# Performance work log

Hardware: AMD Instinct MI355X
Metric: run time of the kernel (lower is better)

The kernel has to match this reference:

```python
import jax, jax.numpy as jnp
import numpy as np

B, T, D_MODEL, H, DH = 4, 2048, 768, 12, 64


def _rope_tables(T, dh):
    # standard rotary frequencies, (T, dh//2)
    inv_freq = 1.0 / (10000.0 ** (np.arange(0, dh, 2, dtype=np.float32) / dh))
    t = np.arange(T, dtype=np.float32)
    ang = np.outer(t, inv_freq)  # (T, dh//2)
    return jnp.asarray(np.cos(ang)), jnp.asarray(np.sin(ang))


def setup_inputs() -> dict:
    key = jax.random.key(0)
    ks = jax.random.split(key, 5)
    scale = 1.0 / np.sqrt(D_MODEL)
    x = jax.random.normal(ks[0], (B, T, D_MODEL), dtype=jnp.float32)
    wq = jax.random.normal(ks[1], (D_MODEL, D_MODEL), dtype=jnp.float32) * scale
    wk = jax.random.normal(ks[2], (D_MODEL, D_MODEL), dtype=jnp.float32) * scale
    wv = jax.random.normal(ks[3], (D_MODEL, D_MODEL), dtype=jnp.float32) * scale
    wo = jax.random.normal(ks[4], (D_MODEL, D_MODEL), dtype=jnp.float32) * scale
    rope_cos, rope_sin = _rope_tables(T, DH)
    return {"x": x, "rope_cos": rope_cos, "rope_sin": rope_sin,
            "wq": wq, "wk": wk, "wv": wv, "wo": wo}


def _apply_rope(x, cos, sin):
    # x: (B, H, T, DH), cos/sin: (T, DH//2) -> interleaved rotation
    t = x.shape[2]
    c = cos[:t][None, None]  # (1,1,T,DH//2)
    s = sin[:t][None, None]
    x1 = x[..., ::2]
    x2 = x[..., 1::2]
    return jnp.stack([x1 * c - x2 * s, x1 * s + x2 * c], axis=-1).reshape(x.shape)


def reference(x, rope_cos, rope_sin, wq, wk, wv, wo):
    b, t, _ = x.shape
    # Linear (torch nn.Linear: y = x @ W.T), split heads -> (B,H,T,DH)
    q = (x @ wq.T).reshape(b, t, H, DH).transpose(0, 2, 1, 3)
    k = (x @ wk.T).reshape(b, t, H, DH).transpose(0, 2, 1, 3)
    v = (x @ wv.T).reshape(b, t, H, DH).transpose(0, 2, 1, 3)
    q = _apply_rope(q, rope_cos, rope_sin)
    k = _apply_rope(k, rope_cos, rope_sin)
    scores = jnp.einsum("bhqd,bhkd->bhqk", q, k) * (DH ** -0.5)
    causal = jnp.tril(jnp.ones((t, t), dtype=bool))  # (T,T)
    scores = jnp.where(causal[None, None], scores, -jnp.inf)
    attn = jax.nn.softmax(scores, axis=-1)
    out = jnp.einsum("bhqk,bhkd->bhqd", attn, v)
    out = out.transpose(0, 2, 1, 3).reshape(b, t, H * DH)
    return out @ wo.T
```

## Files before the change

### kernel.cpp

```cpp
#include <hip/hip_runtime.h>
#include <hip/hip_bf16.h>
#include <math.h>

#define B_ 4
#define T_ 2048
#define DM 768
#define H_ 12
#define DH 64

typedef __attribute__((ext_vector_type(4))) float f32x4;
typedef __attribute__((ext_vector_type(8))) short s16x8;

typedef const __attribute__((address_space(1))) void* gas1_t;
typedef __attribute__((address_space(3))) void* las3_t;

__device__ __forceinline__ ushort f2b(float f) {
  union { float f; unsigned u; } v; v.f = f;
  unsigned u = v.u;
  u += 0x7fffu + ((u >> 16) & 1u);
  return (ushort)(u >> 16);
}
__device__ __forceinline__ unsigned cvt_pk_bf16(float lo, float hi) {
  unsigned r;
  asm("v_cvt_pk_bf16_f32 %0, %1, %2" : "=v"(r) : "v"(lo), "v"(hi));
  return r;
}

__global__ void cvt_all(const float* __restrict__ x,
                        const float* __restrict__ wq, const float* __restrict__ wk,
                        const float* __restrict__ wv, const float* __restrict__ wo,
                        const float* __restrict__ rc, const float* __restrict__ rs,
                        ushort* __restrict__ xb, ushort* __restrict__ wqkv,
                        ushort* __restrict__ wob, float2* __restrict__ cs2) {
  const int bid = blockIdx.x, t = threadIdx.x;
  if (bid < 6144) {
    int i = bid * 256 + t;
    float4 v = ((const float4*)x)[i];
    ushort4 o;
    o.x = f2b(v.x); o.y = f2b(v.y); o.z = f2b(v.z); o.w = f2b(v.w);
    ((ushort4*)xb)[i] = o;
  } else if (bid < 8448) {
    int i = (bid - 6144) * 256 + t;
    int which = i / 147456, j = i - which * 147456;
    const float* src = which == 0 ? wq : which == 1 ? wk : which == 2 ? wv : wo;
    ushort* dst = which < 3 ? wqkv + (size_t)which * 589824 : wob;
    float4 v = ((const float4*)src)[j];
    ushort4 o;
    o.x = f2b(v.x); o.y = f2b(v.y); o.z = f2b(v.z); o.w = f2b(v.w);
    ((ushort4*)dst)[j] = o;
  } else {
    int i = (bid - 8448) * 256 + t;
    cs2[i] = make_float2(rc[i], rs[i]);
  }
}

__global__ __launch_bounds__(256, 3) void gemm_qkv(
    const ushort* __restrict__ A, const ushort* __restrict__ Bw,
    const float2* __restrict__ cs2,
    ushort* __restrict__ Qb, ushort* __restrict__ Kb, ushort* __restrict__ Vt) {
  const int K = 768;
  __shared__ ushort As[128 * 64];
  __shared__ ushort Bs[192 * 64];
  const int bid = blockIdx.x;
  const int xcd = bid & 7;
  const int jj = bid >> 3;
  const int mloc = jj / 12, nn0 = jj - mloc * 12;
  const int m0 = (xcd * 8 + mloc) * 128, n0 = nn0 * 192;
  const int tid = threadIdx.x;
  const int wave = tid >> 6, lane = tid & 63;
  const int wm = (wave >> 1) * 64, wn = (wave & 1) * 96;
  const int quad = lane >> 4, l16 = lane & 15;
  const int tr = tid >> 3;
  const int scb = (tid & 7) ^ (tr & 7);
  const int swz = l16 & 7;

  f32x4 acc[4][6] = {};

  const ushort* ga = A + (size_t)(m0 + tr) * K + scb * 8;
  const ushort* gb = Bw + (size_t)(n0 + tr) * K + scb * 8;

  for (int k0 = 0; k0 < K; k0 += 64) {
#pragma unroll
    for (int p = 0; p < 4; p++)
      __builtin_amdgcn_global_load_lds((gas1_t)(ga + (size_t)(p * 32) * K + k0),
                                       (las3_t)(As + p * 2048 + tid * 8), 16, 0, 0);
#pragma unroll
    for (int p = 0; p < 6; p++)
      __builtin_amdgcn_global_load_lds((gas1_t)(gb + (size_t)(p * 32) * K + k0),
                                       (las3_t)(Bs + p * 2048 + tid * 8), 16, 0, 0);
    __syncthreads();
#pragma unroll
    for (int kk = 0; kk < 2; kk++) {
      s16x8 af[4], bf[6];
#pragma unroll
      for (int i = 0; i < 4; i++) {
        const ushort* ar = As + (wm + i * 16 + l16) * 64;
        af[i] = *(const s16x8*)(ar + (((kk * 4 + quad) ^ swz) * 8));
      }
#pragma unroll
      for (int n = 0; n < 6; n++) {
        const ushort* br = Bs + (wn + n * 16 + l16) * 64;
        bf[n] = *(const s16x8*)(br + (((kk * 4 + quad) ^ swz) * 8));
      }
#pragma unroll
      for (int i = 0; i < 4; i++)
#pragma unroll
        for (int n = 0; n < 6; n++)
          acc[i][n] = __builtin_amdgcn_mfma_f32_16x16x32_bf16(af[i], bf[n], acc[i][n], 0, 0, 0);
    }
    __syncthreads();
  }

  const int sec = n0 / 768;
  if (sec < 2) {
    ushort* dst = sec == 0 ? Qb : Kb;
#pragma unroll
    for (int i = 0; i < 4; i++) {
      int row0 = m0 + wm + i * 16 + quad * 4;
#pragma unroll
      for (int nt = 0; nt < 6; nt++) {
        int col = n0 + wn + nt * 16 + l16;
        int nv = col - sec * 768;
        int h = nv >> 6, d = nv & 63;
        int ip = (d >> 1) & 31;
        float sgn = (d & 1) ? 1.f : -1.f;
#pragma unroll
        for (int r = 0; r < 4; r++) {
          int rrow = row0 + r;
          int t = rrow & (T_ - 1), bb = rrow >> 11;
          float v = acc[i][nt][r];
          float partner = __shfl_xor(v, 1);
          float2 cs = cs2[t * 32 + ip];
          float out = fmaf(v, cs.x, sgn * partner * cs.y);
          dst[((size_t)(bb * H_ + h) * T_ + t) * DH + d] = f2b(out);
        }
      }
    }
  } else {
#pragma unroll
    for (int i = 0; i < 4; i++) {
      int row0 = m0 + wm + i * 16 + quad * 4;
      int t0 = row0 & (T_ - 1), b = row0 >> 11;
#pragma unroll
      for (int nt = 0; nt < 6; nt++) {
        int col = n0 + wn + nt * 16 + l16;
        int nv = col - 1536;
        int h = nv >> 6, d = nv & 63;
        ushort4 pk;
        pk.x = f2b(acc[i][nt][0]); pk.y = f2b(acc[i][nt][1]);
        pk.z = f2b(acc[i][nt][2]); pk.w = f2b(acc[i][nt][3]);
        *(ushort4*)(Vt + ((size_t)(b * H_ + h) * DH + d) * T_ + t0) = pk;
      }
    }
  }
}

__global__ __launch_bounds__(256, 3) void gemm_out(
    const ushort* __restrict__ A, const ushort* __restrict__ Bw, float* __restrict__ C) {
  const int K = 768, N = 768;
  __shared__ ushort As[128 * 64];
  __shared__ ushort Bs[64 * 64];
  const int bid = blockIdx.x;
  const int xcd = bid & 7;
  const int jj = bid >> 3;
  const int mloc = jj / 12, nn0 = jj - mloc * 12;
  const int m0 = (xcd * 8 + mloc) * 128, n0 = nn0 * 64;
  const int tid = threadIdx.x;
  const int wave = tid >> 6, lane = tid & 63;
  const int wm = (wave >> 1) * 64, wn = (wave & 1) * 32;
  const int quad = lane >> 4, l16 = lane & 15;
  const int tr = tid >> 3;
  const int scb = (tid & 7) ^ (tr & 7);
  const int swz = l16 & 7;

  f32x4 acc[4][2] = {};

  const ushort* ga = A + (size_t)(m0 + tr) * K + scb * 8;
  const ushort* gb = Bw + (size_t)(n0 + tr) * K + scb * 8;

  for (int k0 = 0; k0 < K; k0 += 64) {
#pragma unroll
    for (int p = 0; p < 4; p++)
      __builtin_amdgcn_global_load_lds((gas1_t)(ga + (size_t)(p * 32) * K + k0),
                                       (las3_t)(As + p * 2048 + tid * 8), 16, 0, 0);
#pragma unroll
    for (int p = 0; p < 2; p++)
      __builtin_amdgcn_global_load_lds((gas1_t)(gb + (size_t)(p * 32) * K + k0),
                                       (las3_t)(Bs + p * 2048 + tid * 8), 16, 0, 0);
    __syncthreads();
#pragma unroll
    for (int kk = 0; kk < 2; kk++) {
      s16x8 af[4], bf[2];
#pragma unroll
      for (int i = 0; i < 4; i++) {
        const ushort* ar = As + (wm + i * 16 + l16) * 64;
        af[i] = *(const s16x8*)(ar + (((kk * 4 + quad) ^ swz) * 8));
      }
#pragma unroll
      for (int n = 0; n < 2; n++) {
        const ushort* br = Bs + (wn + n * 16 + l16) * 64;
        bf[n] = *(const s16x8*)(br + (((kk * 4 + quad) ^ swz) * 8));
      }
#pragma unroll
      for (int i = 0; i < 4; i++)
#pragma unroll
        for (int n = 0; n < 2; n++)
          acc[i][n] = __builtin_amdgcn_mfma_f32_16x16x32_bf16(af[i], bf[n], acc[i][n], 0, 0, 0);
    }
    __syncthreads();
  }

#pragma unroll
  for (int i = 0; i < 4; i++) {
    int row = m0 + wm + i * 16 + quad * 4;
#pragma unroll
    for (int n = 0; n < 2; n++) {
      int col = n0 + wn + n * 16 + l16;
#pragma unroll
      for (int r = 0; r < 4; r++)
        C[(size_t)(row + r) * N + col] = acc[i][n][r];
    }
  }
}

#define EXP2SCALE 0.18033688f
#define EXP2OFF  17.312340f
__global__ __launch_bounds__(256, 3) void attn(const ushort* __restrict__ Qb, const ushort* __restrict__ Kb,
                                               const ushort* __restrict__ Vt, ushort* __restrict__ Ob) {
  const int bh = blockIdx.x;
  const int p = blockIdx.y;
  const int tid = threadIdx.x, wave = tid >> 6, lane = tid & 63;
  const int quad = lane >> 4, l16 = lane & 15;
  const int b = bh / H_, h = bh % H_;
  const ushort* Qp = Qb + (size_t)bh * T_ * DH;
  const ushort* Kp = Kb + (size_t)bh * T_ * DH;
  const ushort* Vp = Vt + (size_t)bh * DH * T_;

  __shared__ ushort Ks[2][64 * 64];
  __shared__ ushort Vs[2][64 * 64];
  __shared__ ushort P[4][16][72];

  const int srow = tid >> 3;
  const int scbK = (tid & 7) ^ (srow & 7);
  const int swz = (l16 & 7);

#pragma unroll
  for (int phase = 0; phase < 2; phase++) {
    const int tile = phase ? (31 - p) : p;
    const int qb = tile * 64 + wave * 16;

    s16x8 aq0, aq1;
    {
      const ushort* qp = Qp + (size_t)(qb + l16) * DH + quad * 8;
      aq0 = *(const s16x8*)qp;
      aq1 = *(const s16x8*)(qp + 32);
    }
    f32x4 o[4] = {};
    float rsum = 0.f;
    const int ntile = tile + 1;

    __syncthreads();
    {
      const int kv0 = 0;
      __builtin_amdgcn_global_load_lds((gas1_t)(Kp + (size_t)(kv0 + srow) * DH + scbK * 8),
                                       (las3_t)(Ks[0] + tid * 8), 16, 0, 0);
      __builtin_amdgcn_global_load_lds((gas1_t)(Kp + (size_t)(kv0 + srow + 32) * DH + scbK * 8),
                                       (las3_t)(Ks[0] + 2048 + tid * 8), 16, 0, 0);
      __builtin_amdgcn_global_load_lds((gas1_t)(Vp + (size_t)srow * T_ + kv0 + scbK * 8),
                                       (las3_t)(Vs[0] + tid * 8), 16, 0, 0);
      __builtin_amdgcn_global_load_lds((gas1_t)(Vp + (size_t)(srow + 32) * T_ + kv0 + scbK * 8),
                                       (las3_t)(Vs[0] + 2048 + tid * 8), 16, 0, 0);
    }

    for (int c = 0; c < ntile; c++) {
      const int kv0 = c * 64;
      const int cur = c & 1;
      __syncthreads();
      if (c + 1 < ntile) {
        const int kv1 = kv0 + 64, nxt = cur ^ 1;
        __builtin_amdgcn_global_load_lds((gas1_t)(Kp + (size_t)(kv1 + srow) * DH + scbK * 8),
                                         (las3_t)(Ks[nxt] + tid * 8), 16, 0, 0);
        __builtin_amdgcn_global_load_lds((gas1_t)(Kp + (size_t)(kv1 + srow + 32) * DH + scbK * 8),
                                         (las3_t)(Ks[nxt] + 2048 + tid * 8), 16, 0, 0);
        __builtin_amdgcn_global_load_lds((gas1_t)(Vp + (size_t)srow * T_ + kv1 + scbK * 8),
                                         (las3_t)(Vs[nxt] + tid * 8), 16, 0, 0);
        __builtin_amdgcn_global_load_lds((gas1_t)(Vp + (size_t)(srow + 32) * T_ + kv1 + scbK * 8),
                                         (las3_t)(Vs[nxt] + 2048 + tid * 8), 16, 0, 0);
      }

      s16x8 kf[4][2];
#pragma unroll
      for (int nt = 0; nt < 4; nt++) {
        const ushort* kr = Ks[cur] + (nt * 16 + l16) * 64;
        kf[nt][0] = *(const s16x8*)(kr + ((quad ^ swz) * 8));
        kf[nt][1] = *(const s16x8*)(kr + (((4 + quad) ^ swz) * 8));
      }
      s16x8 bv[4][2];
#pragma unroll
      for (int dt = 0; dt < 4; dt++) {
        const ushort* vr = Vs[cur] + (dt * 16 + l16) * 64;
        bv[dt][0] = *(const s16x8*)(vr + ((quad ^ swz) * 8));
        bv[dt][1] = *(const s16x8*)(vr + (((4 + quad) ^ swz) * 8));
      }

      f32x4 s[4] = {};
#pragma unroll
      for (int nt = 0; nt < 4; nt++) {
        s[nt] = __builtin_amdgcn_mfma_f32_16x16x32_bf16(kf[nt][0], aq0, s[nt], 0, 0, 0);
        s[nt] = __builtin_amdgcn_mfma_f32_16x16x32_bf16(kf[nt][1], aq1, s[nt], 0, 0, 0);
      }
      if (c < tile) {
#pragma unroll
        for (int nt = 0; nt < 4; nt++) {
          float p0 = __builtin_amdgcn_exp2f(fmaf(s[nt][0], EXP2SCALE, -EXP2OFF));
          float p1 = __builtin_amdgcn_exp2f(fmaf(s[nt][1], EXP2SCALE, -EXP2OFF));
          float p2 = __builtin_amdgcn_exp2f(fmaf(s[nt][2], EXP2SCALE, -EXP2OFF));
          float p3 = __builtin_amdgcn_exp2f(fmaf(s[nt][3], EXP2SCALE, -EXP2OFF));
          rsum += (p0 + p1) + (p2 + p3);
          uint2 pk;
          pk.x = cvt_pk_bf16(p0, p1);
          pk.y = cvt_pk_bf16(p2, p3);
          *(uint2*)&P[wave][l16][nt * 16 + quad * 4] = pk;
        }
      } else {
        int qi = qb + l16;
#pragma unroll
        for (int nt = 0; nt < 4; nt++) {
          int kvb = kv0 + nt * 16 + quad * 4;
          float pv[4];
#pragma unroll
          for (int r = 0; r < 4; r++)
            pv[r] = (kvb + r <= qi) ? __builtin_amdgcn_exp2f(fmaf(s[nt][r], EXP2SCALE, -EXP2OFF)) : 0.f;
          rsum += (pv[0] + pv[1]) + (pv[2] + pv[3]);
          uint2 pk;
          pk.x = cvt_pk_bf16(pv[0], pv[1]);
          pk.y = cvt_pk_bf16(pv[2], pv[3]);
          *(uint2*)&P[wave][l16][nt * 16 + quad * 4] = pk;
        }
      }
      s16x8 ap0 = *(const s16x8*)&P[wave][l16][quad * 8];
      s16x8 ap1 = *(const s16x8*)&P[wave][l16][32 + quad * 8];
#pragma unroll
      for (int dt = 0; dt < 4; dt++) {
        o[dt] = __builtin_amdgcn_mfma_f32_16x16x32_bf16(ap0, bv[dt][0], o[dt], 0, 0, 0);
        o[dt] = __builtin_amdgcn_mfma_f32_16x16x32_bf16(ap1, bv[dt][1], o[dt], 0, 0, 0);
      }
    }

    rsum += __shfl_xor(rsum, 16);
    rsum += __shfl_xor(rsum, 32);
#pragma unroll
    for (int r = 0; r < 4; r++) {
      float inv = 1.0f / __shfl(rsum, quad * 4 + r);
      int q = qb + quad * 4 + r;
#pragma unroll
      for (int dt = 0; dt < 4; dt++)
        Ob[(size_t)(b * T_ + q) * DM + h * 64 + dt * 16 + l16] = f2b(o[dt][r] * inv);
    }
  }
}

extern "C" void kernel_launch(void* const* d_in, const int* in_sizes, int n_in,
                              void* d_out, int out_size, void* d_ws, size_t ws_size,
                              hipStream_t stream) {
  const float* x = (const float*)d_in[0];
  const float* rc = (const float*)d_in[1];
  const float* rs = (const float*)d_in[2];
  const float* wq = (const float*)d_in[3];
  const float* wk = (const float*)d_in[4];
  const float* wv = (const float*)d_in[5];
  const float* wo = (const float*)d_in[6];

  char* ws = (char*)d_ws;
  ushort* xb   = (ushort*)(ws);
  ushort* wqkv = (ushort*)(ws + 12582912);
  ushort* wob  = (ushort*)(ws + 16121856);
  float2* cs2  = (float2*)(ws + 17301504);
  ushort* Qb   = (ushort*)(ws + 17825792);
  ushort* Kb   = (ushort*)(ws + 30408704);
  ushort* Vt   = (ushort*)(ws + 42991616);
  ushort* Ob   = (ushort*)(ws + 55574528);

  cvt_all<<<8704, 256, 0, stream>>>(x, wq, wk, wv, wo, rc, rs, xb, wqkv, wob, cs2);

  gemm_qkv<<<768, 256, 0, stream>>>(xb, wqkv, cs2, Qb, Kb, Vt);

  attn<<<dim3(48, 16), 256, 0, stream>>>(Qb, Kb, Vt, Ob);

  gemm_out<<<768, 256, 0, stream>>>(Ob, wob, (float*)d_out);
}
```

Measured before the change: 193.4 us.

## Fuse paired causal query tiles into one KV sweep sharing K/V loads

The attention kernel previously processed its two paired query tiles (p and 31-p) in two sequential phases, each streaming K/V from global memory. Now a single KV loop serves both tiles: each loaded K/V block and its LDS fragments feed tile B every iteration and tile A while c <= tileA. This cuts the global-to-LDS traffic and barriers for the shorter tile. The cost is more live registers (two Q fragments, two accumulators), which may pressure occupancy under the 3-blocks launch bound.

```diff
diff --git a/kernel.cpp b/kernel.cpp
--- a/kernel.cpp
+++ b/kernel.cpp
@@ -240,90 +240,92 @@
   __shared__ ushort Vs[2][64 * 64];
   __shared__ ushort P[4][16][72];
 
+  const int tileA = p, tileB = 31 - p;
+  const int qbA = tileA * 64 + wave * 16;
+  const int qbB = tileB * 64 + wave * 16;
+
+  s16x8 aqA0, aqA1, aqB0, aqB1;
+  {
+    const ushort* qp = Qp + (size_t)(qbA + l16) * DH + quad * 8;
+    aqA0 = *(const s16x8*)qp;
+    aqA1 = *(const s16x8*)(qp + 32);
+    const ushort* qp2 = Qp + (size_t)(qbB + l16) * DH + quad * 8;
+    aqB0 = *(const s16x8*)qp2;
+    aqB1 = *(const s16x8*)(qp2 + 32);
+  }
+  f32x4 oA[4] = {}, oB[4] = {};
+  float rsA = 0.f, rsB = 0.f;
+
+  const int ntile = 32 - p;
   const int srow = tid >> 3;
   const int scbK = (tid & 7) ^ (srow & 7);
   const int swz = (l16 & 7);
 
-#pragma unroll
-  for (int phase = 0; phase < 2; phase++) {
-    const int tile = phase ? (31 - p) : p;
-    const int qb = tile * 64 + wave * 16;
-
-    s16x8 aq0, aq1;
+  {
+    const int kv0 = 0;
+    __builtin_amdgcn_global_load_lds((gas1_t)(Kp + (size_t)(kv0 + srow) * DH + scbK * 8),
+                                     (las3_t)(Ks[0] + tid * 8), 16, 0, 0);
+    __builtin_amdgcn_global_load_lds((gas1_t)(Kp + (size_t)(kv0 + srow + 32) * DH + scbK * 8),
+                                     (las3_t)(Ks[0] + 2048 + tid * 8), 16, 0, 0);
+    __builtin_amdgcn_global_load_lds((gas1_t)(Vp + (size_t)srow * T_ + kv0 + scbK * 8),
+                                     (las3_t)(Vs[0] + tid * 8), 16, 0, 0);
+    __builtin_amdgcn_global_load_lds((gas1_t)(Vp + (size_t)(srow + 32) * T_ + kv0 + scbK * 8),
+                                     (las3_t)(Vs[0] + 2048 + tid * 8), 16, 0, 0);
+  }
+
+  for (int c = 0; c < ntile; c++) {
+    const int kv0 = c * 64;
+    const int cur = c & 1;
+    __syncthreads();
+    if (c + 1 < ntile) {
+      const int kv1 = kv0 + 64, nxt = cur ^ 1;
+      __builtin_amdgcn_global_load_lds((gas1_t)(Kp + (size_t)(kv1 + srow) * DH + scbK * 8),
+                                       (las3_t)(Ks[nxt] + tid * 8), 16, 0, 0);
+      __builtin_amdgcn_global_load_lds((gas1_t)(Kp + (size_t)(kv1 + srow + 32) * DH + scbK * 8),
+                                       (las3_t)(Ks[nxt] + 2048 + tid * 8), 16, 0, 0);
+      __builtin_amdgcn_global_load_lds((gas1_t)(Vp + (size_t)srow * T_ + kv1 + scbK * 8),
+                                       (las3_t)(Vs[nxt] + tid * 8), 16, 0, 0);
+      __builtin_amdgcn_global_load_lds((gas1_t)(Vp + (size_t)(srow + 32) * T_ + kv1 + scbK * 8),
+                                       (las3_t)(Vs[nxt] + 2048 + tid * 8), 16, 0, 0);
+    }
+
+    s16x8 kf[4][2];
+#pragma unroll
+    for (int nt = 0; nt < 4; nt++) {
+      const ushort* kr = Ks[cur] + (nt * 16 + l16) * 64;
+      kf[nt][0] = *(const s16x8*)(kr + ((quad ^ swz) * 8));
+      kf[nt][1] = *(const s16x8*)(kr + (((4 + quad) ^ swz) * 8));
+    }
+    s16x8 bv[4][2];
+#pragma unroll
+    for (int dt = 0; dt < 4; dt++) {
+      const ushort* vr = Vs[cur] + (dt * 16 + l16) * 64;
+      bv[dt][0] = *(const s16x8*)(vr + ((quad ^ swz) * 8));
+      bv[dt][1] = *(const s16x8*)(vr + (((4 + quad) ^ swz) * 8));
+    }
+
     {
-      const ushort* qp = Qp + (size_t)(qb + l16) * DH + quad * 8;
-      aq0 = *(const s16x8*)qp;
-      aq1 = *(const s16x8*)(qp + 32);
-    }
-    f32x4 o[4] = {};
-    float rsum = 0.f;
-    const int ntile = tile + 1;
-
-    __syncthreads();
-    {
-      const int kv0 = 0;
-      __builtin_amdgcn_global_load_lds((gas1_t)(Kp + (size_t)(kv0 + srow) * DH + scbK * 8),
-                                       (las3_t)(Ks[0] + tid * 8), 16, 0, 0);
-      __builtin_amdgcn_global_load_lds((gas1_t)(Kp + (size_t)(kv0 + srow + 32) * DH + scbK * 8),
-                                       (las3_t)(Ks[0] + 2048 + tid * 8), 16, 0, 0);
-      __builtin_amdgcn_global_load_lds((gas1_t)(Vp + (size_t)srow * T_ + kv0 + scbK * 8),
-                                       (las3_t)(Vs[0] + tid * 8), 16, 0, 0);
-      __builtin_amdgcn_global_load_lds((gas1_t)(Vp + (size_t)(srow + 32) * T_ + kv0 + scbK * 8),
-                                       (las3_t)(Vs[0] + 2048 + tid * 8), 16, 0, 0);
-    }
-
-    for (int c = 0; c < ntile; c++) {
-      const int kv0 = c * 64;
-      const int cur = c & 1;
-      __syncthreads();
-      if (c + 1 < ntile) {
-        const int kv1 = kv0 + 64, nxt = cur ^ 1;
-        __builtin_amdgcn_global_load_lds((gas1_t)(Kp + (size_t)(kv1 + srow) * DH + scbK * 8),
-                                         (las3_t)(Ks[nxt] + tid * 8), 16, 0, 0);
-        __builtin_amdgcn_global_load_lds((gas1_t)(Kp + (size_t)(kv1 + srow + 32) * DH + scbK * 8),
-                                         (las3_t)(Ks[nxt] + 2048 + tid * 8), 16, 0, 0);
-        __builtin_amdgcn_global_load_lds((gas1_t)(Vp + (size_t)srow * T_ + kv1 + scbK * 8),
-                                         (las3_t)(Vs[nxt] + tid * 8), 16, 0, 0);
-        __builtin_amdgcn_global_load_lds((gas1_t)(Vp + (size_t)(srow + 32) * T_ + kv1 + scbK * 8),
-                                         (las3_t)(Vs[nxt] + 2048 + tid * 8), 16, 0, 0);
-      }
-
-      s16x8 kf[4][2];
+      f32x4 s[4] = {};
 #pragma unroll
       for (int nt = 0; nt < 4; nt++) {
-        const ushort* kr = Ks[cur] + (nt * 16 + l16) * 64;
-        kf[nt][0] = *(const s16x8*)(kr + ((quad ^ swz) * 8));
-        kf[nt][1] = *(const s16x8*)(kr + (((4 + quad) ^ swz) * 8));
-      }
-      s16x8 bv[4][2];
-#pragma unroll
-      for (int dt = 0; dt < 4; dt++) {
-        const ushort* vr = Vs[cur] + (dt * 16 + l16) * 64;
-        bv[dt][0] = *(const s16x8*)(vr + ((quad ^ swz) * 8));
-        bv[dt][1] = *(const s16x8*)(vr + (((4 + quad) ^ swz) * 8));
-      }
-
-      f32x4 s[4] = {};
-#pragma unroll
-      for (int nt = 0; nt < 4; nt++) {
-        s[nt] = __builtin_amdgcn_mfma_f32_16x16x32_bf16(kf[nt][0], aq0, s[nt], 0, 0, 0);
-        s[nt] = __builtin_amdgcn_mfma_f32_16x16x32_bf16(kf[nt][1], aq1, s[nt], 0, 0, 0);
-      }
-      if (c < tile) {
+        s[nt] = __builtin_amdgcn_mfma_f32_16x16x32_bf16(kf[nt][0], aqB0, s[nt], 0, 0, 0);
+        s[nt] = __builtin_amdgcn_mfma_f32_16x16x32_bf16(kf[nt][1], aqB1, s[nt], 0, 0, 0);
+      }
+      if (c < tileB) {
 #pragma unroll
         for (int nt = 0; nt < 4; nt++) {
           float p0 = __builtin_amdgcn_exp2f(fmaf(s[nt][0], EXP2SCALE, -EXP2OFF));
           float p1 = __builtin_amdgcn_exp2f(fmaf(s[nt][1], EXP2SCALE, -EXP2OFF));
           float p2 = __builtin_amdgcn_exp2f(fmaf(s[nt][2], EXP2SCALE, -EXP2OFF));
           float p3 = __builtin_amdgcn_exp2f(fmaf(s[nt][3], EXP2SCALE, -EXP2OFF));
-          rsum += (p0 + p1) + (p2 + p3);
+          rsB += (p0 + p1) + (p2 + p3);
           uint2 pk;
           pk.x = cvt_pk_bf16(p0, p1);
           pk.y = cvt_pk_bf16(p2, p3);
           *(uint2*)&P[wave][l16][nt * 16 + quad * 4] = pk;
         }
       } else {
-        int qi = qb + l16;
+        int qi = qbB + l16;
 #pragma unroll
         for (int nt = 0; nt < 4; nt++) {
           int kvb = kv0 + nt * 16 + quad * 4;
@@ -331,7 +333,7 @@
 #pragma unroll
           for (int r = 0; r < 4; r++)
             pv[r] = (kvb + r <= qi) ? __builtin_amdgcn_exp2f(fmaf(s[nt][r], EXP2SCALE, -EXP2OFF)) : 0.f;
-          rsum += (pv[0] + pv[1]) + (pv[2] + pv[3]);
+          rsB += (pv[0] + pv[1]) + (pv[2] + pv[3]);
           uint2 pk;
           pk.x = cvt_pk_bf16(pv[0], pv[1]);
           pk.y = cvt_pk_bf16(pv[2], pv[3]);
@@ -342,21 +344,76 @@
       s16x8 ap1 = *(const s16x8*)&P[wave][l16][32 + quad * 8];
 #pragma unroll
       for (int dt = 0; dt < 4; dt++) {
-        o[dt] = __builtin_amdgcn_mfma_f32_16x16x32_bf16(ap0, bv[dt][0], o[dt], 0, 0, 0);
-        o[dt] = __builtin_amdgcn_mfma_f32_16x16x32_bf16(ap1, bv[dt][1], o[dt], 0, 0, 0);
-      }
-    }
-
-    rsum += __shfl_xor(rsum, 16);
-    rsum += __shfl_xor(rsum, 32);
-#pragma unroll
-    for (int r = 0; r < 4; r++) {
-      float inv = 1.0f / __shfl(rsum, quad * 4 + r);
-      int q = qb + quad * 4 + r;
-#pragma unroll
-      for (int dt = 0; dt < 4; dt++)
-        Ob[(size_t)(b * T_ + q) * DM + h * 64 + dt * 16 + l16] = f2b(o[dt][r] * inv);
-    }
+        oB[dt] = __builtin_amdgcn_mfma_f32_16x16x32_bf16(ap0, bv[dt][0], oB[dt], 0, 0, 0);
+        oB[dt] = __builtin_amdgcn_mfma_f32_16x16x32_bf16(ap1, bv[dt][1], oB[dt], 0, 0, 0);
+      }
+    }
+
+    if (c <= tileA) {
+      f32x4 s[4] = {};
+#pragma unroll
+      for (int nt = 0; nt < 4; nt++) {
+        s[nt] = __builtin_amdgcn_mfma_f32_16x16x32_bf16(kf[nt][0], aqA0, s[nt], 0, 0, 0);
+        s[nt] = __builtin_amdgcn_mfma_f32_16x16x32_bf16(kf[nt][1], aqA1, s[nt], 0, 0, 0);
+      }
+      if (c < tileA) {
+#pragma unroll
+        for (int nt = 0; nt < 4; nt++) {
+          float p0 = __builtin_amdgcn_exp2f(fmaf(s[nt][0], EXP2SCALE, -EXP2OFF));
+          float p1 = __builtin_amdgcn_exp2f(fmaf(s[nt][1], EXP2SCALE, -EXP2OFF));
+          float p2 = __builtin_amdgcn_exp2f(fmaf(s[nt][2], EXP2SCALE, -EXP2OFF));
+          float p3 = __builtin_amdgcn_exp2f(fmaf(s[nt][3], EXP2SCALE, -EXP2OFF));
+          rsA += (p0 + p1) + (p2 + p3);
+          uint2 pk;
+          pk.x = cvt_pk_bf16(p0, p1);
+          pk.y = cvt_pk_bf16(p2, p3);
+          *(uint2*)&P[wave][l16][nt * 16 + quad * 4] = pk;
+        }
+      } else {
+        int qi = qbA + l16;
+#pragma unroll
+        for (int nt = 0; nt < 4; nt++) {
+          int kvb = kv0 + nt * 16 + quad * 4;
+          float pv[4];
+#pragma unroll
+          for (int r = 0; r < 4; r++)
+            pv[r] = (kvb + r <= qi) ? __builtin_amdgcn_exp2f(fmaf(s[nt][r], EXP2SCALE, -EXP2OFF)) : 0.f;
+          rsA += (pv[0] + pv[1]) + (pv[2] + pv[3]);
+          uint2 pk;
+          pk.x = cvt_pk_bf16(pv[0], pv[1]);
+          pk.y = cvt_pk_bf16(pv[2], pv[3]);
+          *(uint2*)&P[wave][l16][nt * 16 + quad * 4] = pk;
+        }
+      }
+      s16x8 ap0 = *(const s16x8*)&P[wave][l16][quad * 8];
+      s16x8 ap1 = *(const s16x8*)&P[wave][l16][32 + quad * 8];
+#pragma unroll
+      for (int dt = 0; dt < 4; dt++) {
+        oA[dt] = __builtin_amdgcn_mfma_f32_16x16x32_bf16(ap0, bv[dt][0], oA[dt], 0, 0, 0);
+        oA[dt] = __builtin_amdgcn_mfma_f32_16x16x32_bf16(ap1, bv[dt][1], oA[dt], 0, 0, 0);
+      }
+    }
+  }
+
+  rsB += __shfl_xor(rsB, 16);
+  rsB += __shfl_xor(rsB, 32);
+#pragma unroll
+  for (int r = 0; r < 4; r++) {
+    float inv = 1.0f / __shfl(rsB, quad * 4 + r);
+    int q = qbB + quad * 4 + r;
+#pragma unroll
+    for (int dt = 0; dt < 4; dt++)
+      Ob[(size_t)(b * T_ + q) * DM + h * 64 + dt * 16 + l16] = f2b(oB[dt][r] * inv);
+  }
+  rsA += __shfl_xor(rsA, 16);
+  rsA += __shfl_xor(rsA, 32);
+#pragma unroll
+  for (int r = 0; r < 4; r++) {
+    float inv = 1.0f / __shfl(rsA, quad * 4 + r);
+    int q = qbA + quad * 4 + r;
+#pragma unroll
+    for (int dt = 0; dt < 4; dt++)
+      Ob[(size_t)(b * T_ + q) * DM + h * 64 + dt * 16 + l16] = f2b(oA[dt][r] * inv);
   }
 }
 
```

Measured after the change: 179.7 us. 7.1% less time.
